# Kernel optimization log

Hardware: AMD Instinct MI355X
Metric: run time of the kernel (lower is better)

Reference implementation:

```python
import jax, jax.numpy as jnp
import numpy as np

# ---- dims ----
N_NODES = 33      # nodes per graph (33-bus grid)
SEQ     = 24      # time steps per sample
BATCH   = 64      # samples
G       = BATCH * SEQ          # total graphs in the batch
EPG     = 64                   # directed edges per graph
E       = G * EPG              # total edges
N       = G * N_NODES          # total nodes
IN_CH   = 2
HID     = 64
HEADS   = 8
HC      = HID * HEADS          # 512
EDGE_DIM = 3
LSTM1_H = 128
LSTM2_H = 64
N_CLASSES = 4
NEG_SLOPE = 0.2


def setup_inputs() -> dict:
    key = jax.random.key(0)
    ks = jax.random.split(key, 32)
    rng = np.random.default_rng(0)

    # block-structured edge_index: every edge stays inside its own graph
    off = np.repeat(np.arange(G, dtype=np.int64) * N_NODES, EPG)
    src = rng.integers(0, N_NODES, E) + off
    dst = rng.integers(0, N_NODES, E) + off
    edge_index = jnp.asarray(np.stack([src, dst]), dtype=jnp.int32)

    def glorot(k, shape):
        fan = shape[0] + shape[-1]
        s = jnp.sqrt(6.0 / fan).astype(jnp.float32)
        return jax.random.uniform(k, shape, jnp.float32, -s, s)

    inp = dict(
        x=jax.random.normal(ks[0], (N, IN_CH), jnp.float32),
        edge_index=edge_index,
        edge_attr=jax.random.uniform(ks[1], (E, EDGE_DIM), jnp.float32),
        # GATv2 layer 1 (concat=True)
        g1_Wl=glorot(ks[2], (IN_CH, HC)),
        g1_Wr=glorot(ks[3], (IN_CH, HC)),
        g1_We=glorot(ks[4], (EDGE_DIM, HC)),
        g1_att=glorot(ks[5], (HEADS, HID)),
        g1_b=jnp.zeros((HC,), jnp.float32),
        # GATv2 layer 2 (concat=False -> head mean)
        g2_Wl=glorot(ks[6], (HC, HC)),
        g2_Wr=glorot(ks[7], (HC, HC)),
        g2_We=glorot(ks[8], (EDGE_DIM, HC)),
        g2_att=glorot(ks[9], (HEADS, HID)),
        g2_b=jnp.zeros((HID,), jnp.float32),
        # LSTM1: input 33*64=2112 -> 128, gates ordered (i,f,g,o)
        l1_Wih=0.05 * jax.random.normal(ks[10], (4 * LSTM1_H, N_NODES * HID), jnp.float32),
        l1_Whh=0.05 * jax.random.normal(ks[11], (4 * LSTM1_H, LSTM1_H), jnp.float32),
        l1_bih=jnp.zeros((4 * LSTM1_H,), jnp.float32),
        l1_bhh=jnp.zeros((4 * LSTM1_H,), jnp.float32),
        # LSTM2: 128 -> 64
        l2_Wih=0.05 * jax.random.normal(ks[12], (4 * LSTM2_H, LSTM1_H), jnp.float32),
        l2_Whh=0.05 * jax.random.normal(ks[13], (4 * LSTM2_H, LSTM2_H), jnp.float32),
        l2_bih=jnp.zeros((4 * LSTM2_H,), jnp.float32),
        l2_bhh=jnp.zeros((4 * LSTM2_H,), jnp.float32),
        # FC 64 -> n_classes
        fc_W=0.05 * jax.random.normal(ks[14], (N_CLASSES, LSTM2_H), jnp.float32),
        fc_b=jnp.zeros((N_CLASSES,), jnp.float32),
    )
    return inp


def _gatv2(x, edge_attr, src, dst, Wl, Wr, We, att, b, concat):
    """PyG GATv2Conv with edge_dim, add_self_loops semantics omitted is NOT used:
    we follow the message math: m = leaky_relu(xl[src]+xr[dst]+We@e),
    alpha = segment_softmax(<m,att>, dst), out = scatter_add(alpha * xl[src])."""
    n = x.shape[0]
    xl = (x @ Wl).reshape(n, HEADS, HID)      # [N,H,C]
    xr = (x @ Wr).reshape(n, HEADS, HID)
    em = (edge_attr @ We).reshape(-1, HEADS, HID)  # [E,H,C]
    m = jax.nn.leaky_relu(xl[src] + xr[dst] + em, NEG_SLOPE)
    logits = jnp.einsum('ehc,hc->eh', m, att)          # [E,H]
    mx = jax.ops.segment_max(logits, dst, num_segments=n)   # [N,H]
    ex = jnp.exp(logits - mx[dst])
    den = jax.ops.segment_sum(ex, dst, num_segments=n)
    alpha = ex / (den[dst] + 1e-16)                    # [E,H]
    out = jax.ops.segment_sum(xl[src] * alpha[:, :, None], dst, num_segments=n)  # [N,H,C]
    out = out.reshape(n, HC) if concat else out.mean(axis=1)
    return out + b


def _lstm(x, Wih, Whh, bih, bhh, hsz):
    B = x.shape[0]
    h0 = jnp.zeros((B, hsz), x.dtype)
    c0 = jnp.zeros((B, hsz), x.dtype)

    def step(carry, xt):
        h, c = carry
        gates = xt @ Wih.T + h @ Whh.T + bih + bhh
        i, f, g, o = jnp.split(gates, 4, axis=-1)
        i = jax.nn.sigmoid(i); f = jax.nn.sigmoid(f)
        g = jnp.tanh(g);       o = jax.nn.sigmoid(o)
        c = f * c + i * g
        h = o * jnp.tanh(c)
        return (h, c), h

    _, ys = jax.lax.scan(step, (h0, c0), x.transpose(1, 0, 2))  # [T,B,H]
    return ys.transpose(1, 0, 2)


def reference(x, edge_index, edge_attr,
              g1_Wl, g1_Wr, g1_We, g1_att, g1_b,
              g2_Wl, g2_Wr, g2_We, g2_att, g2_b,
              l1_Wih, l1_Whh, l1_bih, l1_bhh,
              l2_Wih, l2_Whh, l2_bih, l2_bhh,
              fc_W, fc_b):
    src, dst = edge_index[0], edge_index[1]
    h = jax.nn.elu(_gatv2(x, edge_attr, src, dst, g1_Wl, g1_Wr, g1_We, g1_att, g1_b, True))
    h = jax.nn.elu(_gatv2(h, edge_attr, src, dst, g2_Wl, g2_Wr, g2_We, g2_att, g2_b, False))
    seq = h.reshape(BATCH, SEQ, N_NODES * HID)          # [B,T,2112]
    seq = _lstm(seq, l1_Wih, l1_Whh, l1_bih, l1_bhh, LSTM1_H)
    seq = _lstm(seq, l2_Wih, l2_Whh, l2_bih, l2_bhh, LSTM2_H)
    last = seq[:, -1, :]                                 # [B,64]
    return last @ fc_W.T + fc_b                          # [B,n_classes]
```

## Files before the change

### kernel.cpp

```cpp
#include <hip/hip_runtime.h>
#include <math.h>

#define N_NODES 33
#define SEQ 24
#define BATCH 64
#define G_GRAPHS (BATCH * SEQ)
#define EPG 64
#define E_EDGES (G_GRAPHS * EPG)
#define N_TOTAL (G_GRAPHS * N_NODES)
#define HID 64
#define HEADS 8
#define HC (HID * HEADS)
#define LSTM1_H 128
#define LSTM2_H 64
#define NEG_SLOPE 0.2f
#define CONV_BLOCKS (128 + 264)

__device__ __forceinline__ float sigmoidf_(float x) { return 1.f / (1.f + expf(-x)); }
__device__ __forceinline__ float eluf_(float x) { return x > 0.f ? x : expm1f(x); }
__device__ __forceinline__ float lreluf_(float x) { return x > 0.f ? x : NEG_SLOPE * x; }

typedef __attribute__((ext_vector_type(4))) float f32x4;
typedef _Float16 half_t;
typedef __attribute__((ext_vector_type(8))) _Float16 halfx8;

__device__ __forceinline__ void gl2lds16(const void* g, void* l) {
  __builtin_amdgcn_global_load_lds(
      (__attribute__((address_space(1))) const unsigned int*)g,
      (__attribute__((address_space(3))) unsigned int*)l, 16, 0, 0);
}

__global__ __launch_bounds__(512) void gat1_kernel(
    const float* __restrict__ x, const int* __restrict__ src, const int* __restrict__ dst,
    const float* __restrict__ ea, const float* __restrict__ Wl, const float* __restrict__ Wr,
    const float* __restrict__ We, const float* __restrict__ att, const float* __restrict__ bias,
    half_t* __restrict__ h1, int g0, int gat_blocks,
    const float* __restrict__ g2Wl, const float* __restrict__ g2Wr,
    half_t* __restrict__ B2, const float* __restrict__ W1, half_t* __restrict__ W1f) {
  const int tid = threadIdx.x;

  __shared__ alignas(16) float Wl_s[2 * 512];
  __shared__ alignas(16) float Wr_s[2 * 512];
  __shared__ alignas(16) float We_s[3 * 512];
  __shared__ alignas(16) float att_s[512];
  __shared__ float xs0_s[N_NODES + 1], xs1_s[N_NODES + 1];
  __shared__ float easX[EPG], easY[EPG], easZ[EPG];
  __shared__ float logit_s[HEADS * 65];
  __shared__ int sloc[EPG], dloc[EPG], deg[N_NODES], start[N_NODES], fill[N_NODES], elist[EPG];
  __shared__ float tr[64 * 65];

  if ((int)blockIdx.x >= gat_blocks) {
    int cb = blockIdx.x - gat_blocks;
    if (cb < 128) {
      int kt = cb & 7, nt = cb >> 3;
      int k0 = kt * 64, n0 = nt * 64;
      int r = tid >> 6, c = tid & 63;
      #pragma unroll
      for (int rr = 0; rr < 8; ++rr) {
        int kl = rr * 8 + r;
        int n = n0 + c;
        float v = (n < 512) ? g2Wl[(size_t)(k0 + kl) * 512 + n]
                            : g2Wr[(size_t)(k0 + kl) * 512 + n - 512];
        tr[kl * 65 + c] = v;
      }
      __syncthreads();
      #pragma unroll
      for (int rr = 0; rr < 8; ++rr) {
        int nl = rr * 8 + r;
        B2[(size_t)(n0 + nl) * 512 + k0 + c] = (half_t)tr[c * 65 + nl];
      }
    } else {
      int base = (cb - 128) * 4096 + tid;
      #pragma unroll
      for (int i = 0; i < 8; ++i) {
        int idx = base + i * 512;
        if (idx < 512 * 2112) W1f[idx] = (half_t)W1[idx];
      }
    }
    return;
  }

  const int g = g0 + blockIdx.x;
  const int nb = g * N_NODES, eb = g * EPG;
  const int lb = blockIdx.x * N_NODES;

  for (int i = tid; i < 1024; i += 512) { Wl_s[i] = Wl[i]; Wr_s[i] = Wr[i]; }
  for (int i = tid; i < 1536; i += 512) We_s[i] = We[i];
  if (tid < 512) att_s[tid] = att[tid];
  if (tid < 2 * N_NODES) {
    float v = x[nb * 2 + tid];
    if (tid & 1) xs1_s[tid >> 1] = v; else xs0_s[tid >> 1] = v;
  }
  if (tid < EPG) {
    easX[tid] = ea[(eb + tid) * 3 + 0];
    easY[tid] = ea[(eb + tid) * 3 + 1];
    easZ[tid] = ea[(eb + tid) * 3 + 2];
    sloc[tid] = src[eb + tid] - nb;
    dloc[tid] = dst[eb + tid] - nb;
  }
  if (tid < N_NODES) { deg[tid] = 0; fill[tid] = 0; }
  __syncthreads();
  if (tid < EPG) atomicAdd(&deg[dloc[tid]], 1);
  __syncthreads();
  if (tid == 0) { int a = 0; for (int n = 0; n < N_NODES; ++n) { start[n] = a; a += deg[n]; } }
  __syncthreads();
  if (tid < EPG) { int d = dloc[tid]; int p = atomicAdd(&fill[d], 1); elist[start[d] + p] = tid; }

  {
    int h = tid >> 6, e = tid & 63;
    int s = sloc[e], d = dloc[e];
    float xs0 = xs0_s[s], xs1 = xs1_s[s], xd0 = xs0_s[d], xd1 = xs1_s[d];
    float e0 = easX[e], e1 = easY[e], e2 = easZ[e];
    float acc = 0.f;
    int base = h * 64;
    #pragma unroll
    for (int c4 = 0; c4 < 16; ++c4) {
      int j = base + c4 * 4;
      f32x4 wl0 = *(const f32x4*)(Wl_s + j);
      f32x4 wl1 = *(const f32x4*)(Wl_s + 512 + j);
      f32x4 wr0 = *(const f32x4*)(Wr_s + j);
      f32x4 wr1 = *(const f32x4*)(Wr_s + 512 + j);
      f32x4 we0 = *(const f32x4*)(We_s + j);
      f32x4 we1 = *(const f32x4*)(We_s + 512 + j);
      f32x4 we2 = *(const f32x4*)(We_s + 1024 + j);
      f32x4 at  = *(const f32x4*)(att_s + j);
      #pragma unroll
      for (int q = 0; q < 4; ++q) {
        float v = xs0 * wl0[q] + xs1 * wl1[q]
                + xd0 * wr0[q] + xd1 * wr1[q]
                + e0 * we0[q] + e1 * we1[q] + e2 * we2[q];
        acc += lreluf_(v) * at[q];
      }
    }
    logit_s[h * 65 + e] = acc;
  }
  __syncthreads();

  {
    int h = tid >> 6, n = tid & 63;
    if (n < N_NODES) {
      int s0 = start[n], dn = deg[n];
      float mx = -1e30f;
      for (int i = 0; i < dn; ++i) mx = fmaxf(mx, logit_s[h * 65 + elist[s0 + i]]);
      float den = 0.f;
      for (int i = 0; i < dn; ++i) den += expf(logit_s[h * 65 + elist[s0 + i]] - mx);
      float inv = 1.f / (den + 1e-16f);
      for (int i = 0; i < dn; ++i) {
        int e = elist[s0 + i];
        logit_s[h * 65 + e] = expf(logit_s[h * 65 + e] - mx) * inv;
      }
    }
  }
  __syncthreads();

  for (int t = tid; t < N_NODES * 64; t += 512) {
    int n = t >> 6, jb = t & 63;
    int j0 = jb * 8, h = jb >> 3;
    f32x4 wa0 = *(const f32x4*)(Wl_s + j0);
    f32x4 wa1 = *(const f32x4*)(Wl_s + j0 + 4);
    f32x4 wb0 = *(const f32x4*)(Wl_s + 512 + j0);
    f32x4 wb1 = *(const f32x4*)(Wl_s + 512 + j0 + 4);
    float acc[8] = {};
    int s0 = start[n], dn = deg[n];
    for (int i = 0; i < dn; ++i) {
      int e = elist[s0 + i]; int s = sloc[e];
      float a = logit_s[h * 65 + e];
      float ax0 = a * xs0_s[s], ax1 = a * xs1_s[s];
      #pragma unroll
      for (int q = 0; q < 4; ++q) {
        acc[q]     += ax0 * wa0[q] + ax1 * wb0[q];
        acc[4 + q] += ax0 * wa1[q] + ax1 * wb1[q];
      }
    }
    f32x4 b0 = *(const f32x4*)(bias + j0);
    f32x4 b1 = *(const f32x4*)(bias + j0 + 4);
    halfx8 vh;
    #pragma unroll
    for (int cc = 0; cc < 8; ++cc) {
      float bb = (cc < 4) ? b0[cc] : b1[cc - 4];
      vh[cc] = (half_t)eluf_(acc[cc] + bb);
    }
    *(halfx8*)(h1 + (size_t)(lb + n) * HC + j0) = vh;
  }
}

__global__ __launch_bounds__(512, 2) void gemm256(
    const half_t* __restrict__ A, const half_t* __restrict__ B,
    half_t* __restrict__ C, int M) {
  __shared__ alignas(16) half_t lds[65536];

  const int R = M >> 8;
  int b = blockIdx.x;
  int xcd = b & 7, q = b >> 3;
  int ct = q & 3, rg = q >> 2;
  int r = rg * 8 + xcd;
  if (r >= R) return;

  const int tid = threadIdx.x;
  const int wave = tid >> 6, lane = tid & 63;
  const int wm = wave >> 2, wn = wave & 3;
  const int bm = r << 8, bn = ct << 8;

  const int rA = lane >> 2;
  const int swzS = (rA & 3) ^ ((rA >> 2) & 3);
  const int cA = ((lane & 3) ^ swzS) * 8;

  const int fr = lane & 15;
  const int fs = (fr & 3) ^ ((fr >> 2) & 3);
  const int fk = ((lane >> 4) ^ fs) * 8;

  f32x4 acc[8][4];
  #pragma unroll
  for (int tm = 0; tm < 8; ++tm)
    #pragma unroll
    for (int tn = 0; tn < 4; ++tn) acc[tm][tn] = {0.f, 0.f, 0.f, 0.f};

  auto stage = [&](int kt, int slot) {
    half_t* As = lds + slot * 16384;
    half_t* Bs = As + 8192;
    const int koff = kt * 32 + cA;
    #pragma unroll
    for (int i = 0; i < 2; ++i) {
      int row = i * 128 + wave * 16;
      gl2lds16(A + (size_t)(bm + row + rA) * 512 + koff, As + row * 32);
      gl2lds16(B + (size_t)(bn + row + rA) * 512 + koff, Bs + row * 32);
    }
  };

  stage(0, 0);
  stage(1, 1);
  stage(2, 2);

  for (int kt = 0; kt < 16; ++kt) {
    if (kt < 14)       asm volatile("s_waitcnt vmcnt(8)" ::: "memory");
    else if (kt == 14) asm volatile("s_waitcnt vmcnt(4)" ::: "memory");
    else               asm volatile("s_waitcnt vmcnt(0)" ::: "memory");
    __builtin_amdgcn_s_barrier();
    asm volatile("" ::: "memory");

    if (kt + 3 < 16) stage(kt + 3, (kt + 3) & 3);

    const half_t* As = lds + (kt & 3) * 16384;
    const half_t* Bs = As + 8192;

    halfx8 bf[4];
    #pragma unroll
    for (int tn = 0; tn < 4; ++tn)
      bf[tn] = *(const halfx8*)(Bs + (wn * 64 + tn * 16 + fr) * 32 + fk);

    __builtin_amdgcn_s_setprio(1);
    #pragma unroll
    for (int tm = 0; tm < 8; ++tm) {
      halfx8 af = *(const halfx8*)(As + (wm * 128 + tm * 16 + fr) * 32 + fk);
      #pragma unroll
      for (int tn = 0; tn < 4; ++tn)
        acc[tm][tn] = __builtin_amdgcn_mfma_f32_16x16x32_f16(af, bf[tn], acc[tm][tn], 0, 0, 0);
    }
    __builtin_amdgcn_s_setprio(0);
  }

  half_t* Cs = lds;
  const int rq = (lane >> 4) * 4;
  const int cl0 = lane & 15;
  #pragma unroll 1
  for (int mh = 0; mh < 2; ++mh) {
    __syncthreads();
    if (wm == mh) {
      #pragma unroll
      for (int tm = 0; tm < 8; ++tm)
        #pragma unroll
        for (int tn = 0; tn < 4; ++tn) {
          int cl = wn * 64 + tn * 16 + cl0;
          #pragma unroll
          for (int rr = 0; rr < 4; ++rr)
            Cs[(tm * 16 + rq + rr) * 264 + cl] = (half_t)acc[tm][tn][rr];
        }
    }
    __syncthreads();
    #pragma unroll
    for (int i = 0; i < 8; ++i) {
      int rr2 = i * 16 + (tid >> 5);
      int cc = (tid & 31) * 8;
      halfx8 v = *(const halfx8*)(Cs + rr2 * 264 + cc);
      *(halfx8*)(C + (size_t)(bm + mh * 128 + rr2) * 1024 + bn + cc) = v;
    }
  }
}

__global__ __launch_bounds__(256) void gemm_f16_splitk(
    const half_t* __restrict__ A, const half_t* __restrict__ B,
    float* __restrict__ Cp, const float* __restrict__ bias1, const float* __restrict__ bias2,
    int M, int N) {
  constexpr int SA = 2112;
  __shared__ half_t lds[(64 + 64) * 64];
  half_t* A_s = lds;
  half_t* B_s = A_s + 2 * 64 * 32;

  const int part = blockIdx.y;
  const int koff = part ? 576 + (part - 1) * 512 : 0;
  const int kend = part ? 512 : 576;
  const half_t* Ap = A + koff;
  const half_t* Bp = B + koff;
  float* C = Cp + (size_t)part * M * N;

  const int R = M / 64, NT = N / 64;
  int b = blockIdx.x;
  int xcd = b & 7, q = b >> 3;
  int ct = q % NT, rg = q / NT;
  int r = rg * 8 + xcd;
  if (r >= R) return;

  const int tid = threadIdx.x;
  const int wave = tid >> 6, lane = tid & 63;
  const int wm = wave >> 1, wn = wave & 1;
  const int bm = r * 64, bn = ct * 64;

  const int rA = lane >> 2;
  const int swz = (rA & 3) ^ ((rA >> 2) & 3);
  const int cA = ((lane & 3) ^ swz) * 8;

  f32x4 acc[2][2];
  #pragma unroll
  for (int tm = 0; tm < 2; ++tm)
    #pragma unroll
    for (int tn = 0; tn < 2; ++tn) acc[tm][tn] = {0.f, 0.f, 0.f, 0.f};

  for (int k0 = 0; k0 < kend; k0 += 64) {
    #pragma unroll
    for (int p = 0; p < 2; ++p) {
      int kk = k0 + p * 32;
      int row = wave * 16;
      gl2lds16(Ap + (size_t)(bm + row + rA) * SA + kk + cA,
               A_s + p * 64 * 32 + row * 32);
      gl2lds16(Bp + (size_t)(bn + row + rA) * SA + kk + cA,
               B_s + p * 64 * 32 + row * 32);
    }
    __syncthreads();
    const int fr = lane & 15;
    const int fs = (fr & 3) ^ ((fr >> 2) & 3);
    const int fk = ((lane >> 4) ^ fs) * 8;
    #pragma unroll
    for (int p = 0; p < 2; ++p) {
      const int pA = p * 64 * 32, pB = p * 64 * 32;
      halfx8 af[2], bf[2];
      #pragma unroll
      for (int tm = 0; tm < 2; ++tm) {
        int rr = (wm * 2 + tm) * 16 + fr;
        af[tm] = *(const halfx8*)(A_s + pA + rr * 32 + fk);
      }
      #pragma unroll
      for (int tn = 0; tn < 2; ++tn) {
        int rr = (wn * 2 + tn) * 16 + fr;
        bf[tn] = *(const halfx8*)(B_s + pB + rr * 32 + fk);
      }
      #pragma unroll
      for (int tm = 0; tm < 2; ++tm)
        #pragma unroll
        for (int tn = 0; tn < 2; ++tn)
          acc[tm][tn] = __builtin_amdgcn_mfma_f32_16x16x32_f16(af[tm], bf[tn], acc[tm][tn], 0, 0, 0);
    }
    __syncthreads();
  }

  const int col0 = lane & 15, rq = (lane >> 4) * 4;
  #pragma unroll
  for (int tm = 0; tm < 2; ++tm)
    #pragma unroll
    for (int tn = 0; tn < 2; ++tn) {
      int col = bn + (wn * 2 + tn) * 16 + col0;
      float badd = (part == 0) ? (bias1[col] + bias2[col]) : 0.f;
      #pragma unroll
      for (int rr = 0; rr < 4; ++rr) {
        int row = bm + (wm * 2 + tm) * 16 + rq + rr;
        C[(size_t)row * N + col] = acc[tm][tn][rr] + badd;
      }
    }
}

__global__ __launch_bounds__(512) void gat2_kernel(
    const half_t* __restrict__ xlr, const int* __restrict__ src, const int* __restrict__ dst,
    const float* __restrict__ ea, const float* __restrict__ We,
    const float* __restrict__ att, const float* __restrict__ bias,
    half_t* __restrict__ h2, int g0) {
  __shared__ alignas(16) float We_s[3 * 512];
  __shared__ alignas(16) float att_s[512];
  __shared__ float b_s[HID];
  __shared__ float easX[EPG], easY[EPG], easZ[EPG];
  __shared__ float logit_s[HEADS * 65];
  __shared__ int sloc[EPG], dloc[EPG], deg[N_NODES], start[N_NODES], fill[N_NODES], elist[EPG];

  const int g = g0 + blockIdx.x, tid = threadIdx.x;
  const int nb = g * N_NODES, eb = g * EPG;
  const int lb = blockIdx.x * N_NODES;
  const int wave = tid >> 6, lane = tid & 63;

  for (int i = tid; i < 1536; i += 512) We_s[i] = We[i];
  if (tid < 512) att_s[tid] = att[tid];
  if (tid < HID) b_s[tid] = bias[tid];
  if (tid < EPG) {
    easX[tid] = ea[(eb + tid) * 3 + 0];
    easY[tid] = ea[(eb + tid) * 3 + 1];
    easZ[tid] = ea[(eb + tid) * 3 + 2];
    sloc[tid] = src[eb + tid] - nb;
    dloc[tid] = dst[eb + tid] - nb;
  }
  if (tid < N_NODES) { deg[tid] = 0; fill[tid] = 0; }
  __syncthreads();
  if (tid < EPG) atomicAdd(&deg[dloc[tid]], 1);
  __syncthreads();
  if (tid == 0) { int a = 0; for (int n = 0; n < N_NODES; ++n) { start[n] = a; a += deg[n]; } }
  __syncthreads();
  if (tid < EPG) { int d = dloc[tid]; int p = atomicAdd(&fill[d], 1); elist[start[d] + p] = tid; }
  __syncthreads();

  const int j0 = lane * 8;
  float w0[8], w1[8], w2[8], at8[8];
  #pragma unroll
  for (int q = 0; q < 8; ++q) {
    w0[q] = We_s[j0 + q];
    w1[q] = We_s[512 + j0 + q];
    w2[q] = We_s[1024 + j0 + q];
    at8[q] = att_s[j0 + q];
  }

  for (int e = wave; e < EPG; e += 8) {
    int s = sloc[e], d = dloc[e];
    halfx8 xlv = *((const halfx8*)(xlr + (size_t)(lb + s) * 1024) + lane);
    halfx8 xrv = *((const halfx8*)(xlr + (size_t)(lb + d) * 1024 + 512) + lane);
    float e0 = easX[e], e1 = easY[e], e2 = easZ[e];
    float acc = 0.f;
    #pragma unroll
    for (int q = 0; q < 8; ++q) {
      float v = (float)xlv[q] + (float)xrv[q] + e0 * w0[q] + e1 * w1[q] + e2 * w2[q];
      acc += lreluf_(v) * at8[q];
    }
    acc += __shfl_xor(acc, 1, 64);
    acc += __shfl_xor(acc, 2, 64);
    acc += __shfl_xor(acc, 4, 64);
    if ((lane & 7) == 0) logit_s[(lane >> 3) * 65 + e] = acc;
  }
  __syncthreads();

  {
    int h = tid >> 6, n = tid & 63;
    if (n < N_NODES) {
      int s0 = start[n], dn = deg[n];
      float mx = -1e30f;
      for (int i = 0; i < dn; ++i) mx = fmaxf(mx, logit_s[h * 65 + elist[s0 + i]]);
      float den = 0.f;
      for (int i = 0; i < dn; ++i) den += expf(logit_s[h * 65 + elist[s0 + i]] - mx);
      float inv = 1.f / (den + 1e-16f);
      for (int i = 0; i < dn; ++i) {
        int e = elist[s0 + i];
        logit_s[h * 65 + e] = expf(logit_s[h * 65 + e] - mx) * inv;
      }
    }
  }
  __syncthreads();

  for (int n = wave; n < N_NODES; n += 8) {
    float acc = 0.f;
    int s0 = start[n], dn = deg[n];
    for (int i = 0; i < dn; ++i) {
      int e = elist[s0 + i], s = sloc[e];
      const half_t* row = xlr + (size_t)(lb + s) * 1024 + lane;
      #pragma unroll
      for (int h = 0; h < 8; ++h)
        acc += logit_s[h * 65 + e] * (float)row[h * 64];
    }
    float v = eluf_(acc * 0.125f + b_s[lane]);
    h2[(size_t)(nb + n) * HID + lane] = (half_t)v;
  }
}

__global__ __launch_bounds__(1024, 4) void lstm_all(
    const float* __restrict__ X0, const float* __restrict__ X1,
    const float* __restrict__ X2p, const float* __restrict__ X3,
    const float* __restrict__ Whh1,
    const float* __restrict__ Wih2, const float* __restrict__ bih2,
    const float* __restrict__ bhh2, const float* __restrict__ Whh2,
    const float* __restrict__ fcW, const float* __restrict__ fcb,
    float* __restrict__ out) {
  __shared__ float hs1[LSTM1_H], cs1[LSTM1_H], p1[512], gs1[512];
  __shared__ float Y1s[SEQ][LSTM1_H];
  __shared__ float hs2[LSTM2_H], cs2[LSTM2_H], p2[4 * 256], gs2[256];
  const int tid = threadIdx.x, b = blockIdx.x;
  const int j = tid & 511, half = tid >> 9;

  float4 w1[16];
  {
    const float4* wp = (const float4*)(Whh1 + (size_t)j * LSTM1_H + half * 64);
    #pragma unroll
    for (int q = 0; q < 16; ++q) w1[q] = wp[q];
  }
  if (tid < LSTM1_H) { hs1[tid] = 0.f; cs1[tid] = 0.f; }
  __syncthreads();
  for (int t = 0; t < SEQ; ++t) {
    const float* hb = hs1 + half * 64;
    float acc = 0.f;
    #pragma unroll
    for (int q = 0; q < 16; ++q) {
      acc += w1[q].x * hb[4 * q] + w1[q].y * hb[4 * q + 1]
           + w1[q].z * hb[4 * q + 2] + w1[q].w * hb[4 * q + 3];
    }
    if (half) p1[j] = acc;
    __syncthreads();
    if (!half) {
      size_t xo = ((size_t)b * SEQ + t) * 512 + j;
      gs1[j] = acc + p1[j] + X0[xo] + X1[xo] + X2p[xo] + X3[xo];
    }
    __syncthreads();
    if (tid < LSTM1_H) {
      float ig = sigmoidf_(gs1[tid]);
      float fg = sigmoidf_(gs1[LSTM1_H + tid]);
      float gg = tanhf(gs1[2 * LSTM1_H + tid]);
      float og = sigmoidf_(gs1[3 * LSTM1_H + tid]);
      float c = fg * cs1[tid] + ig * gg;
      cs1[tid] = c;
      float h = og * tanhf(c);
      hs1[tid] = h;
      Y1s[t][tid] = h;
    }
    __syncthreads();
  }

  const int j2 = tid & 255, qt = tid >> 8;
  float4 w2x[8], w2h[4];
  {
    const float4* wxp = (const float4*)(Wih2 + (size_t)j2 * LSTM1_H + qt * 32);
    #pragma unroll
    for (int q = 0; q < 8; ++q) w2x[q] = wxp[q];
    const float4* whp = (const float4*)(Whh2 + (size_t)j2 * LSTM2_H + qt * 16);
    #pragma unroll
    for (int q = 0; q < 4; ++q) w2h[q] = whp[q];
  }
  if (tid < LSTM2_H) { hs2[tid] = 0.f; cs2[tid] = 0.f; }
  __syncthreads();
  for (int t = 0; t < SEQ; ++t) {
    const float* y = Y1s[t] + qt * 32;
    const float* hb = hs2 + qt * 16;
    float acc = 0.f;
    #pragma unroll
    for (int q = 0; q < 8; ++q) {
      acc += w2x[q].x * y[4 * q] + w2x[q].y * y[4 * q + 1]
           + w2x[q].z * y[4 * q + 2] + w2x[q].w * y[4 * q + 3];
    }
    #pragma unroll
    for (int q = 0; q < 4; ++q) {
      acc += w2h[q].x * hb[4 * q] + w2h[q].y * hb[4 * q + 1]
           + w2h[q].z * hb[4 * q + 2] + w2h[q].w * hb[4 * q + 3];
    }
    p2[qt * 256 + j2] = acc;
    __syncthreads();
    if (qt == 0)
      gs2[j2] = p2[j2] + p2[256 + j2] + p2[512 + j2] + p2[768 + j2]
              + bih2[j2] + bhh2[j2];
    __syncthreads();
    if (tid < LSTM2_H) {
      float ig = sigmoidf_(gs2[tid]);
      float fg = sigmoidf_(gs2[LSTM2_H + tid]);
      float gg = tanhf(gs2[2 * LSTM2_H + tid]);
      float og = sigmoidf_(gs2[3 * LSTM2_H + tid]);
      float c = fg * cs2[tid] + ig * gg;
      cs2[tid] = c;
      hs2[tid] = og * tanhf(c);
    }
    __syncthreads();
  }
  if (tid < 4) {
    float acc = fcb[tid];
    #pragma unroll
    for (int k = 0; k < LSTM2_H; ++k) acc += fcW[tid * LSTM2_H + k] * hs2[k];
    out[b * 4 + tid] = acc;
  }
}

extern "C" void kernel_launch(void* const* d_in, const int* in_sizes, int n_in,
                              void* d_out, int out_size, void* d_ws, size_t ws_size,
                              hipStream_t stream) {
  const float* x       = (const float*)d_in[0];
  const int*   eidx    = (const int*)d_in[1];
  const float* eattr   = (const float*)d_in[2];
  const float* g1_Wl   = (const float*)d_in[3];
  const float* g1_Wr   = (const float*)d_in[4];
  const float* g1_We   = (const float*)d_in[5];
  const float* g1_att  = (const float*)d_in[6];
  const float* g1_b    = (const float*)d_in[7];
  const float* g2_Wl   = (const float*)d_in[8];
  const float* g2_Wr   = (const float*)d_in[9];
  const float* g2_We   = (const float*)d_in[10];
  const float* g2_att  = (const float*)d_in[11];
  const float* g2_b    = (const float*)d_in[12];
  const float* l1_Wih  = (const float*)d_in[13];
  const float* l1_Whh  = (const float*)d_in[14];
  const float* l1_bih  = (const float*)d_in[15];
  const float* l1_bhh  = (const float*)d_in[16];
  const float* l2_Wih  = (const float*)d_in[17];
  const float* l2_Whh  = (const float*)d_in[18];
  const float* l2_bih  = (const float*)d_in[19];
  const float* l2_bhh  = (const float*)d_in[20];
  const float* fc_W    = (const float*)d_in[21];
  const float* fc_b    = (const float*)d_in[22];
  float* out = (float*)d_out;

  const int* src = eidx;
  const int* dst = eidx + E_EDGES;

  const int cand[4] = {1, 2, 3, 6};
  int nchunks = 0;
  half_t *h1 = nullptr, *xlr2c = nullptr, *h2 = nullptr, *B2 = nullptr, *W1f = nullptr;
  float *X1p = nullptr;
  int chunk_g = 0, chunk_n = 0;
  for (int ci = 0; ci < 4; ++ci) {
    int C = cand[ci];
    int CG = G_GRAPHS / C, CN = CG * N_NODES;
    char* p = (char*)d_ws;
    auto alloc = [&](size_t bytes) { char* r = p; p += (bytes + 255) & ~(size_t)255; return r; };
    half_t* t_h1    = (half_t*)alloc((size_t)CN * HC * 2);
    half_t* t_xlr2c = (half_t*)alloc((size_t)CN * 1024 * 2);
    half_t* t_h2    = (half_t*)alloc((size_t)G_GRAPHS * 2112 * 2);
    half_t* t_B2    = (half_t*)alloc((size_t)1024 * 512 * 2);
    half_t* t_W1f   = (half_t*)alloc((size_t)512 * 2112 * 2);
    float*  t_X1p   = (float*)alloc((size_t)4 * G_GRAPHS * 512 * 4);
    if ((size_t)(p - (char*)d_ws) <= ws_size) {
      nchunks = C; chunk_g = CG; chunk_n = CN;
      h1 = t_h1; xlr2c = t_xlr2c; h2 = t_h2; B2 = t_B2; W1f = t_W1f;
      X1p = t_X1p;
      break;
    }
  }
  if (nchunks == 0) return;

  for (int c = 0; c < nchunks; ++c) {
    int g0 = c * chunk_g;
    int extra = (c == 0) ? CONV_BLOCKS : 0;
    gat1_kernel<<<chunk_g + extra, 512, 0, stream>>>(
        x, src, dst, eattr, g1_Wl, g1_Wr, g1_We, g1_att, g1_b, h1, g0, chunk_g,
        g2_Wl, g2_Wr, B2, l1_Wih, W1f);
    int R = chunk_n / 256;
    int gblocks = 8 * ((R + 7) / 8) * 4;
    gemm256<<<gblocks, 512, 0, stream>>>(h1, B2, xlr2c, chunk_n);
    gat2_kernel<<<chunk_g, 512, 0, stream>>>(xlr2c, src, dst, eattr, g2_We,
                                             g2_att, g2_b, h2, g0);
  }

  {
    dim3 grid(192, 4);
    gemm_f16_splitk<<<grid, 256, 0, stream>>>(h2, W1f, X1p, l1_bih, l1_bhh,
                                              G_GRAPHS, 512);
  }

  {
    size_t PS = (size_t)G_GRAPHS * 512;
    lstm_all<<<BATCH, 1024, 0, stream>>>(X1p, X1p + PS, X1p + 2 * PS, X1p + 3 * PS,
                                         l1_Whh, l2_Wih, l2_bih, l2_bhh, l2_Whh,
                                         fc_W, fc_b, out);
  }
}
```

Baseline: 359.5 us.

## Restructure GAT2 projection GEMM into 8-phase ping-pong pipeline with BK=64

```diff
diff --git a/kernel.cpp b/kernel.cpp
--- a/kernel.cpp
+++ b/kernel.cpp
@@ -184,7 +184,39 @@
   }
 }
 
-__global__ __launch_bounds__(512, 2) void gemm256(
+#define PHASE_BAR() do { asm volatile("" ::: "memory"); \
+  __builtin_amdgcn_s_barrier(); asm volatile("" ::: "memory"); } while (0)
+
+#define LDA8(S, rr, kc) \
+  (*(const halfx8*)((S) + (rr) * 64 + (((kc) ^ ((rr) & 7)) << 3)))
+
+#define READ_B(Bs)                                                        \
+  _Pragma("unroll")                                                       \
+  for (int tn = 0; tn < 4; ++tn)                                          \
+    _Pragma("unroll")                                                     \
+    for (int ks = 0; ks < 2; ++ks)                                        \
+      bf[tn][ks] = LDA8(Bs, wn * 64 + tn * 16 + fr, ks * 4 + kq);
+
+#define READ_A(As, q)                                                     \
+  _Pragma("unroll")                                                       \
+  for (int tl = 0; tl < 2; ++tl)                                          \
+    _Pragma("unroll")                                                     \
+    for (int ks = 0; ks < 2; ++ks)                                        \
+      af[tl][ks] = LDA8(As, wm * 128 + ((q) * 2 + tl) * 16 + fr, ks * 4 + kq);
+
+#define MFMA_Q(q)                                                         \
+  __builtin_amdgcn_s_setprio(1);                                          \
+  _Pragma("unroll")                                                       \
+  for (int ks = 0; ks < 2; ++ks)                                          \
+    _Pragma("unroll")                                                     \
+    for (int tl = 0; tl < 2; ++tl)                                        \
+      _Pragma("unroll")                                                   \
+      for (int tn = 0; tn < 4; ++tn)                                      \
+        acc[(q) * 2 + tl][tn] = __builtin_amdgcn_mfma_f32_16x16x32_f16(   \
+            af[tl][ks], bf[tn][ks], acc[(q) * 2 + tl][tn], 0, 0, 0);      \
+  __builtin_amdgcn_s_setprio(0);
+
+__global__ __launch_bounds__(512, 2) void gemm256_8p(
     const half_t* __restrict__ A, const half_t* __restrict__ B,
     half_t* __restrict__ C, int M) {
   __shared__ alignas(16) half_t lds[65536];
@@ -201,13 +233,19 @@
   const int wm = wave >> 2, wn = wave & 3;
   const int bm = r << 8, bn = ct << 8;
 
-  const int rA = lane >> 2;
-  const int swzS = (rA & 3) ^ ((rA >> 2) & 3);
-  const int cA = ((lane & 3) ^ swzS) * 8;
-
+  const int rl = lane >> 3;
+  const int gc = ((lane & 7) ^ rl) << 3;
   const int fr = lane & 15;
-  const int fs = (fr & 3) ^ ((fr >> 2) & 3);
-  const int fk = ((lane >> 4) ^ fs) * 8;
+  const int kq = lane >> 4;
+
+  half_t* A0w = lds;
+  half_t* B0w = lds + 16384;
+  half_t* A1w = lds + 32768;
+  half_t* B1w = lds + 49152;
+  const half_t* A0s = A0w;
+  const half_t* B0s = B0w;
+  const half_t* A1s = A1w;
+  const half_t* B1s = B1w;
 
   f32x4 acc[8][4];
   #pragma unroll
@@ -215,48 +253,62 @@
     #pragma unroll
     for (int tn = 0; tn < 4; ++tn) acc[tm][tn] = {0.f, 0.f, 0.f, 0.f};
 
-  auto stage = [&](int kt, int slot) {
-    half_t* As = lds + slot * 16384;
-    half_t* Bs = As + 8192;
-    const int koff = kt * 32 + cA;
-    #pragma unroll
-    for (int i = 0; i < 2; ++i) {
-      int row = i * 128 + wave * 16;
-      gl2lds16(A + (size_t)(bm + row + rA) * 512 + koff, As + row * 32);
-      gl2lds16(B + (size_t)(bn + row + rA) * 512 + koff, Bs + row * 32);
-    }
+  auto stage_ht = [&](const half_t* __restrict__ G, int rowbase, int kt, int h,
+                      half_t* Ls) {
+    const int r0 = h * 128 + wave * 16;
+    const half_t* gp = G + (size_t)(rowbase + r0 + rl) * 512 + kt * 64 + gc;
+    gl2lds16(gp, Ls + r0 * 64);
+    gl2lds16(gp + (size_t)8 * 512, Ls + (r0 + 8) * 64);
   };
 
-  stage(0, 0);
-  stage(1, 1);
-  stage(2, 2);
-
-  for (int kt = 0; kt < 16; ++kt) {
-    if (kt < 14)       asm volatile("s_waitcnt vmcnt(8)" ::: "memory");
-    else if (kt == 14) asm volatile("s_waitcnt vmcnt(4)" ::: "memory");
-    else               asm volatile("s_waitcnt vmcnt(0)" ::: "memory");
-    __builtin_amdgcn_s_barrier();
-    asm volatile("" ::: "memory");
-
-    if (kt + 3 < 16) stage(kt + 3, (kt + 3) & 3);
-
-    const half_t* As = lds + (kt & 3) * 16384;
-    const half_t* Bs = As + 8192;
-
-    halfx8 bf[4];
-    #pragma unroll
-    for (int tn = 0; tn < 4; ++tn)
-      bf[tn] = *(const halfx8*)(Bs + (wn * 64 + tn * 16 + fr) * 32 + fk);
-
-    __builtin_amdgcn_s_setprio(1);
-    #pragma unroll
-    for (int tm = 0; tm < 8; ++tm) {
-      halfx8 af = *(const halfx8*)(As + (wm * 128 + tm * 16 + fr) * 32 + fk);
-      #pragma unroll
-      for (int tn = 0; tn < 4; ++tn)
-        acc[tm][tn] = __builtin_amdgcn_mfma_f32_16x16x32_f16(af, bf[tn], acc[tm][tn], 0, 0, 0);
-    }
-    __builtin_amdgcn_s_setprio(0);
+  stage_ht(B, bn, 0, 0, B0w);
+  stage_ht(B, bn, 0, 1, B0w);
+  stage_ht(A, bm, 0, 0, A0w);
+  stage_ht(A, bm, 0, 1, A0w);
+  stage_ht(B, bn, 1, 0, B1w);
+  stage_ht(B, bn, 1, 1, B1w);
+  asm volatile("s_waitcnt vmcnt(4)" ::: "memory");
+  PHASE_BAR();
+
+  #pragma unroll
+  for (int j = 0; j < 4; ++j) {
+    const int t1 = 2 * j + 1;
+    const bool nl = (j < 3);
+    halfx8 bf[4][2], af[2][2];
+
+    READ_B(B0s); READ_A(A0s, 0);
+    stage_ht(A, bm, t1, 0, A1w);
+    PHASE_BAR(); MFMA_Q(0); PHASE_BAR();
+    READ_A(A0s, 1);
+    stage_ht(A, bm, t1, 1, A1w);
+    PHASE_BAR(); MFMA_Q(1); PHASE_BAR();
+    READ_A(A0s, 2);
+    if (nl) stage_ht(B, bn, t1 + 1, 0, B0w);
+    PHASE_BAR(); MFMA_Q(2); PHASE_BAR();
+    READ_A(A0s, 3);
+    if (nl) {
+      stage_ht(B, bn, t1 + 1, 1, B0w);
+      asm volatile("s_waitcnt vmcnt(4)" ::: "memory");
+    } else {
+      asm volatile("s_waitcnt vmcnt(0)" ::: "memory");
+    }
+    PHASE_BAR(); MFMA_Q(3); PHASE_BAR();
+
+    READ_B(B1s); READ_A(A1s, 0);
+    if (nl) stage_ht(A, bm, t1 + 1, 0, A0w);
+    PHASE_BAR(); MFMA_Q(0); PHASE_BAR();
+    READ_A(A1s, 1);
+    if (nl) stage_ht(A, bm, t1 + 1, 1, A0w);
+    PHASE_BAR(); MFMA_Q(1); PHASE_BAR();
+    READ_A(A1s, 2);
+    if (nl) stage_ht(B, bn, t1 + 2, 0, B1w);
+    PHASE_BAR(); MFMA_Q(2); PHASE_BAR();
+    READ_A(A1s, 3);
+    if (nl) {
+      stage_ht(B, bn, t1 + 2, 1, B1w);
+      asm volatile("s_waitcnt vmcnt(4)" ::: "memory");
+    }
+    PHASE_BAR(); MFMA_Q(3); PHASE_BAR();
   }
 
   half_t* Cs = lds;
@@ -639,7 +691,7 @@
         g2_Wl, g2_Wr, B2, l1_Wih, W1f);
     int R = chunk_n / 256;
     int gblocks = 8 * ((R + 7) / 8) * 4;
-    gemm256<<<gblocks, 512, 0, stream>>>(h1, B2, xlr2c, chunk_n);
+    gemm256_8p<<<gblocks, 512, 0, stream>>>(h1, B2, xlr2c, chunk_n);
     gat2_kernel<<<chunk_g, 512, 0, stream>>>(xlr2c, src, dst, eattr, g2_We,
                                              g2_att, g2_b, h2, g0);
   }
```

Result: no change. 354.2 us (-1.5%).

## Restructure layer-2 GEMM to 128x256 tiles with split-phase double-buffered pipeline

Applied to the files above, without the earlier changes.

```diff
diff --git a/kernel.cpp b/kernel.cpp
--- a/kernel.cpp
+++ b/kernel.cpp
@@ -184,106 +184,143 @@
   }
 }
 
-__global__ __launch_bounds__(512, 2) void gemm256(
+#define PHASE_BAR() do { asm volatile("" ::: "memory"); \
+  __builtin_amdgcn_s_barrier(); asm volatile("" ::: "memory"); } while (0)
+
+#define LDA8(S, rr, c) \
+  (*(const halfx8*)((S) + (rr) * 64 + ((((c) ^ ((rr) & 7))) << 3)))
+
+__global__ __launch_bounds__(512, 2) void gemm128x256(
     const half_t* __restrict__ A, const half_t* __restrict__ B,
     half_t* __restrict__ C, int M) {
-  __shared__ alignas(16) half_t lds[65536];
-
-  const int R = M >> 8;
-  int b = blockIdx.x;
-  int xcd = b & 7, q = b >> 3;
-  int ct = q & 3, rg = q >> 2;
-  int r = rg * 8 + xcd;
-  if (r >= R) return;
+  __shared__ alignas(16) half_t lds[49152];
+
+  const int R = M >> 7;
+  const int nwg = R * 4;
+  int bid = blockIdx.x;
+  const int cpx = nwg >> 3;
+  int swz = (bid & 7) * cpx + (bid >> 3);
+  const int ct = swz & 3, r = swz >> 2;
 
   const int tid = threadIdx.x;
   const int wave = tid >> 6, lane = tid & 63;
   const int wm = wave >> 2, wn = wave & 3;
-  const int bm = r << 8, bn = ct << 8;
-
-  const int rA = lane >> 2;
-  const int swzS = (rA & 3) ^ ((rA >> 2) & 3);
-  const int cA = ((lane & 3) ^ swzS) * 8;
-
+  const int bm = r << 7, bn = ct << 8;
+
+  const int rl = lane >> 3;
+  const int gc = ((lane & 7) ^ rl) << 3;
   const int fr = lane & 15;
-  const int fs = (fr & 3) ^ ((fr >> 2) & 3);
-  const int fk = ((lane >> 4) ^ fs) * 8;
-
-  f32x4 acc[8][4];
+  const int kq = lane >> 4;
+
+  half_t* const Ab0 = lds;
+  half_t* const Ab1 = lds + 8192;
+  half_t* const Bb0 = lds + 16384;
+  half_t* const Bb1 = lds + 32768;
+
+  f32x4 acc[4][4];
   #pragma unroll
-  for (int tm = 0; tm < 8; ++tm)
+  for (int tm = 0; tm < 4; ++tm)
     #pragma unroll
     for (int tn = 0; tn < 4; ++tn) acc[tm][tn] = {0.f, 0.f, 0.f, 0.f};
 
-  auto stage = [&](int kt, int slot) {
-    half_t* As = lds + slot * 16384;
-    half_t* Bs = As + 8192;
-    const int koff = kt * 32 + cA;
+  auto stageA = [&](int kt) {
+    half_t* Ls = (kt & 1) ? Ab1 : Ab0;
     #pragma unroll
     for (int i = 0; i < 2; ++i) {
-      int row = i * 128 + wave * 16;
-      gl2lds16(A + (size_t)(bm + row + rA) * 512 + koff, As + row * 32);
-      gl2lds16(B + (size_t)(bn + row + rA) * 512 + koff, Bs + row * 32);
+      int r0 = i * 64 + wave * 8;
+      gl2lds16(A + (size_t)(bm + r0 + rl) * 512 + kt * 64 + gc, Ls + r0 * 64);
     }
   };
-
-  stage(0, 0);
-  stage(1, 1);
-  stage(2, 2);
-
-  for (int kt = 0; kt < 16; ++kt) {
-    if (kt < 14)       asm volatile("s_waitcnt vmcnt(8)" ::: "memory");
-    else if (kt == 14) asm volatile("s_waitcnt vmcnt(4)" ::: "memory");
-    else               asm volatile("s_waitcnt vmcnt(0)" ::: "memory");
-    __builtin_amdgcn_s_barrier();
-    asm volatile("" ::: "memory");
-
-    if (kt + 3 < 16) stage(kt + 3, (kt + 3) & 3);
-
-    const half_t* As = lds + (kt & 3) * 16384;
-    const half_t* Bs = As + 8192;
-
-    halfx8 bf[4];
+  auto stageB = [&](int kt) {
+    half_t* Ls = (kt & 1) ? Bb1 : Bb0;
+    #pragma unroll
+    for (int i = 0; i < 4; ++i) {
+      int r0 = i * 64 + wave * 8;
+      gl2lds16(B + (size_t)(bn + r0 + rl) * 512 + kt * 64 + gc, Ls + r0 * 64);
+    }
+  };
+
+  stageB(0);
+  stageA(0);
+  stageB(1);
+  asm volatile("s_waitcnt vmcnt(4)" ::: "memory");
+  PHASE_BAR();
+
+  #pragma unroll
+  for (int t = 0; t < 8; ++t) {
+    const half_t* As = (t & 1) ? Ab1 : Ab0;
+    const half_t* Bs = (t & 1) ? Bb1 : Bb0;
+    halfx8 bf[4][2], afA[2][2], afB[2][2];
+
     #pragma unroll
     for (int tn = 0; tn < 4; ++tn)
-      bf[tn] = *(const halfx8*)(Bs + (wn * 64 + tn * 16 + fr) * 32 + fk);
-
+      #pragma unroll
+      for (int ks = 0; ks < 2; ++ks)
+        bf[tn][ks] = LDA8(Bs, wn * 64 + tn * 16 + fr, ks * 4 + kq);
+    #pragma unroll
+    for (int tl = 0; tl < 2; ++tl)
+      #pragma unroll
+      for (int ks = 0; ks < 2; ++ks)
+        afA[tl][ks] = LDA8(As, wm * 64 + tl * 16 + fr, ks * 4 + kq);
+    if (t < 7) stageA(t + 1);
+    PHASE_BAR();
     __builtin_amdgcn_s_setprio(1);
     #pragma unroll
-    for (int tm = 0; tm < 8; ++tm) {
-      halfx8 af = *(const halfx8*)(As + (wm * 128 + tm * 16 + fr) * 32 + fk);
-      #pragma unroll
-      for (int tn = 0; tn < 4; ++tn)
-        acc[tm][tn] = __builtin_amdgcn_mfma_f32_16x16x32_f16(af, bf[tn], acc[tm][tn], 0, 0, 0);
-    }
+    for (int ks = 0; ks < 2; ++ks)
+      #pragma unroll
+      for (int tl = 0; tl < 2; ++tl)
+        #pragma unroll
+        for (int tn = 0; tn < 4; ++tn)
+          acc[tl][tn] = __builtin_amdgcn_mfma_f32_16x16x32_f16(
+              afA[tl][ks], bf[tn][ks], acc[tl][tn], 0, 0, 0);
     __builtin_amdgcn_s_setprio(0);
+    PHASE_BAR();
+
+    #pragma unroll
+    for (int tl = 0; tl < 2; ++tl)
+      #pragma unroll
+      for (int ks = 0; ks < 2; ++ks)
+        afB[tl][ks] = LDA8(As, wm * 64 + (2 + tl) * 16 + fr, ks * 4 + kq);
+    if (t < 6) {
+      stageB(t + 2);
+      asm volatile("s_waitcnt vmcnt(4)" ::: "memory");
+    } else if (t == 6) {
+      asm volatile("s_waitcnt vmcnt(0)" ::: "memory");
+    }
+    PHASE_BAR();
+    __builtin_amdgcn_s_setprio(1);
+    #pragma unroll
+    for (int ks = 0; ks < 2; ++ks)
+      #pragma unroll
+      for (int tl = 0; tl < 2; ++tl)
+        #pragma unroll
+        for (int tn = 0; tn < 4; ++tn)
+          acc[2 + tl][tn] = __builtin_amdgcn_mfma_f32_16x16x32_f16(
+              afB[tl][ks], bf[tn][ks], acc[2 + tl][tn], 0, 0, 0);
+    __builtin_amdgcn_s_setprio(0);
+    PHASE_BAR();
   }
 
   half_t* Cs = lds;
   const int rq = (lane >> 4) * 4;
   const int cl0 = lane & 15;
-  #pragma unroll 1
-  for (int mh = 0; mh < 2; ++mh) {
-    __syncthreads();
-    if (wm == mh) {
-      #pragma unroll
-      for (int tm = 0; tm < 8; ++tm)
-        #pragma unroll
-        for (int tn = 0; tn < 4; ++tn) {
-          int cl = wn * 64 + tn * 16 + cl0;
-          #pragma unroll
-          for (int rr = 0; rr < 4; ++rr)
-            Cs[(tm * 16 + rq + rr) * 264 + cl] = (half_t)acc[tm][tn][rr];
-        }
-    }
-    __syncthreads();
-    #pragma unroll
-    for (int i = 0; i < 8; ++i) {
-      int rr2 = i * 16 + (tid >> 5);
-      int cc = (tid & 31) * 8;
-      halfx8 v = *(const halfx8*)(Cs + rr2 * 264 + cc);
-      *(halfx8*)(C + (size_t)(bm + mh * 128 + rr2) * 1024 + bn + cc) = v;
-    }
+  __syncthreads();
+  #pragma unroll
+  for (int tm = 0; tm < 4; ++tm)
+    #pragma unroll
+    for (int tn = 0; tn < 4; ++tn) {
+      int cl = wn * 64 + tn * 16 + cl0;
+      #pragma unroll
+      for (int rr = 0; rr < 4; ++rr)
+        Cs[(wm * 64 + tm * 16 + rq + rr) * 264 + cl] = (half_t)acc[tm][tn][rr];
+    }
+  __syncthreads();
+  #pragma unroll
+  for (int i = 0; i < 8; ++i) {
+    int row = i * 16 + (tid >> 5);
+    int col = (tid & 31) * 8;
+    halfx8 v = *(const halfx8*)(Cs + row * 264 + col);
+    *(halfx8*)(C + (size_t)(bm + row) * 1024 + bn + col) = v;
   }
 }
 
@@ -637,9 +674,8 @@
     gat1_kernel<<<chunk_g + extra, 512, 0, stream>>>(
         x, src, dst, eattr, g1_Wl, g1_Wr, g1_We, g1_att, g1_b, h1, g0, chunk_g,
         g2_Wl, g2_Wr, B2, l1_Wih, W1f);
-    int R = chunk_n / 256;
-    int gblocks = 8 * ((R + 7) / 8) * 4;
-    gemm256<<<gblocks, 512, 0, stream>>>(h1, B2, xlr2c, chunk_n);
+    int gblocks = (chunk_n / 128) * 4;
+    gemm128x256<<<gblocks, 512, 0, stream>>>(h1, B2, xlr2c, chunk_n);
     gat2_kernel<<<chunk_g, 512, 0, stream>>>(xlr2c, src, dst, eattr, g2_We,
                                              g2_att, g2_b, h2, g0);
   }
```

Measured after the change: 346.8 us. 3.5% less time.

## Replace 256x256 pipelined GEMM with 128x128 tile single-buffer GEMM

Applied to the files above, without the earlier changes.

```diff
diff --git a/kernel.cpp b/kernel.cpp
--- a/kernel.cpp
+++ b/kernel.cpp
@@ -184,106 +184,91 @@
   }
 }
 
-__global__ __launch_bounds__(512, 2) void gemm256(
+#define LDA8(S, rr, c) \
+  (*(const halfx8*)((S) + (rr) * 64 + ((((c) ^ ((rr) & 7))) << 3)))
+
+__global__ __launch_bounds__(256, 4) void gemm_m97(
     const half_t* __restrict__ A, const half_t* __restrict__ B,
     half_t* __restrict__ C, int M) {
-  __shared__ alignas(16) half_t lds[65536];
-
-  const int R = M >> 8;
-  int b = blockIdx.x;
-  int xcd = b & 7, q = b >> 3;
-  int ct = q & 3, rg = q >> 2;
-  int r = rg * 8 + xcd;
-  if (r >= R) return;
+  __shared__ alignas(16) half_t lds[128 * 132];
+
+  half_t* const As = lds;
+  half_t* const Bs = lds + 8192;
+
+  const int R = M >> 7;
+  const int nwg = R * 8;
+  const int cpx = nwg >> 3;
+  const int bid = blockIdx.x;
+  const int swz = (bid & 7) * cpx + (bid >> 3);
+  const int ct = swz & 7, r = swz >> 3;
 
   const int tid = threadIdx.x;
   const int wave = tid >> 6, lane = tid & 63;
-  const int wm = wave >> 2, wn = wave & 3;
-  const int bm = r << 8, bn = ct << 8;
-
-  const int rA = lane >> 2;
-  const int swzS = (rA & 3) ^ ((rA >> 2) & 3);
-  const int cA = ((lane & 3) ^ swzS) * 8;
-
+  const int wm = wave >> 1, wn = wave & 1;
+  const int bm = r << 7, bn = ct << 7;
+
+  const int rl = lane >> 3;
+  const int gc = ((lane & 7) ^ rl) << 3;
   const int fr = lane & 15;
-  const int fs = (fr & 3) ^ ((fr >> 2) & 3);
-  const int fk = ((lane >> 4) ^ fs) * 8;
-
-  f32x4 acc[8][4];
+  const int kq = lane >> 4;
+
+  f32x4 acc[4][4];
   #pragma unroll
-  for (int tm = 0; tm < 8; ++tm)
+  for (int tm = 0; tm < 4; ++tm)
     #pragma unroll
     for (int tn = 0; tn < 4; ++tn) acc[tm][tn] = {0.f, 0.f, 0.f, 0.f};
 
-  auto stage = [&](int kt, int slot) {
-    half_t* As = lds + slot * 16384;
-    half_t* Bs = As + 8192;
-    const int koff = kt * 32 + cA;
-    #pragma unroll
-    for (int i = 0; i < 2; ++i) {
-      int row = i * 128 + wave * 16;
-      gl2lds16(A + (size_t)(bm + row + rA) * 512 + koff, As + row * 32);
-      gl2lds16(B + (size_t)(bn + row + rA) * 512 + koff, Bs + row * 32);
-    }
-  };
-
-  stage(0, 0);
-  stage(1, 1);
-  stage(2, 2);
-
-  for (int kt = 0; kt < 16; ++kt) {
-    if (kt < 14)       asm volatile("s_waitcnt vmcnt(8)" ::: "memory");
-    else if (kt == 14) asm volatile("s_waitcnt vmcnt(4)" ::: "memory");
-    else               asm volatile("s_waitcnt vmcnt(0)" ::: "memory");
-    __builtin_amdgcn_s_barrier();
-    asm volatile("" ::: "memory");
-
-    if (kt + 3 < 16) stage(kt + 3, (kt + 3) & 3);
-
-    const half_t* As = lds + (kt & 3) * 16384;
-    const half_t* Bs = As + 8192;
-
-    halfx8 bf[4];
-    #pragma unroll
-    for (int tn = 0; tn < 4; ++tn)
-      bf[tn] = *(const halfx8*)(Bs + (wn * 64 + tn * 16 + fr) * 32 + fk);
-
-    __builtin_amdgcn_s_setprio(1);
-    #pragma unroll
-    for (int tm = 0; tm < 8; ++tm) {
-      halfx8 af = *(const halfx8*)(As + (wm * 128 + tm * 16 + fr) * 32 + fk);
+  for (int t = 0; t < 8; ++t) {
+    #pragma unroll
+    for (int i = 0; i < 4; ++i) {
+      int r0 = i * 32 + wave * 8;
+      gl2lds16(A + (size_t)(bm + r0 + rl) * 512 + t * 64 + gc, As + r0 * 64);
+    }
+    #pragma unroll
+    for (int i = 0; i < 4; ++i) {
+      int r0 = i * 32 + wave * 8;
+      gl2lds16(B + (size_t)(bn + r0 + rl) * 512 + t * 64 + gc, Bs + r0 * 64);
+    }
+    __syncthreads();
+
+    #pragma unroll
+    for (int ks = 0; ks < 2; ++ks) {
+      halfx8 af[4], bf[4];
+      #pragma unroll
+      for (int tm = 0; tm < 4; ++tm)
+        af[tm] = LDA8(As, wm * 64 + tm * 16 + fr, ks * 4 + kq);
       #pragma unroll
       for (int tn = 0; tn < 4; ++tn)
-        acc[tm][tn] = __builtin_amdgcn_mfma_f32_16x16x32_f16(af, bf[tn], acc[tm][tn], 0, 0, 0);
-    }
-    __builtin_amdgcn_s_setprio(0);
+        bf[tn] = LDA8(Bs, wn * 64 + tn * 16 + fr, ks * 4 + kq);
+      #pragma unroll
+      for (int tm = 0; tm < 4; ++tm)
+        #pragma unroll
+        for (int tn = 0; tn < 4; ++tn)
+          acc[tm][tn] = __builtin_amdgcn_mfma_f32_16x16x32_f16(
+              af[tm], bf[tn], acc[tm][tn], 0, 0, 0);
+    }
+    __syncthreads();
   }
 
   half_t* Cs = lds;
-  const int rq = (lane >> 4) * 4;
+  const int rq4 = (lane >> 4) * 4;
   const int cl0 = lane & 15;
-  #pragma unroll 1
-  for (int mh = 0; mh < 2; ++mh) {
-    __syncthreads();
-    if (wm == mh) {
-      #pragma unroll
-      for (int tm = 0; tm < 8; ++tm)
-        #pragma unroll
-        for (int tn = 0; tn < 4; ++tn) {
-          int cl = wn * 64 + tn * 16 + cl0;
-          #pragma unroll
-          for (int rr = 0; rr < 4; ++rr)
-            Cs[(tm * 16 + rq + rr) * 264 + cl] = (half_t)acc[tm][tn][rr];
-        }
-    }
-    __syncthreads();
-    #pragma unroll
-    for (int i = 0; i < 8; ++i) {
-      int rr2 = i * 16 + (tid >> 5);
-      int cc = (tid & 31) * 8;
-      halfx8 v = *(const halfx8*)(Cs + rr2 * 264 + cc);
-      *(halfx8*)(C + (size_t)(bm + mh * 128 + rr2) * 1024 + bn + cc) = v;
-    }
+  #pragma unroll
+  for (int tm = 0; tm < 4; ++tm)
+    #pragma unroll
+    for (int tn = 0; tn < 4; ++tn) {
+      int cl = wn * 64 + tn * 16 + cl0;
+      #pragma unroll
+      for (int rr = 0; rr < 4; ++rr)
+        Cs[(wm * 64 + tm * 16 + rq4 + rr) * 132 + cl] = (half_t)acc[tm][tn][rr];
+    }
+  __syncthreads();
+  #pragma unroll
+  for (int pass = 0; pass < 8; ++pass) {
+    int row = pass * 16 + (tid >> 4);
+    int col = (tid & 15) * 8;
+    halfx8 v = *(const halfx8*)(Cs + row * 132 + col);
+    *(halfx8*)(C + (size_t)(bm + row) * 1024 + bn + col) = v;
   }
 }
 
@@ -637,9 +622,8 @@
     gat1_kernel<<<chunk_g + extra, 512, 0, stream>>>(
         x, src, dst, eattr, g1_Wl, g1_Wr, g1_We, g1_att, g1_b, h1, g0, chunk_g,
         g2_Wl, g2_Wr, B2, l1_Wih, W1f);
-    int R = chunk_n / 256;
-    int gblocks = 8 * ((R + 7) / 8) * 4;
-    gemm256<<<gblocks, 512, 0, stream>>>(h1, B2, xlr2c, chunk_n);
+    int gblocks = (chunk_n / 128) * 8;
+    gemm_m97<<<gblocks, 256, 0, stream>>>(h1, B2, xlr2c, chunk_n);
     gat2_kernel<<<chunk_g, 512, 0, stream>>>(xlr2c, src, dst, eattr, g2_We,
                                              g2_att, g2_b, h2, g0);
   }
```

Measured after the change: 340.9 us. -5.2%, faster.
